# Kernel optimization log

Hardware: AMD Instinct MI355X
Metric: run time of the kernel (lower is better)

The kernel has to match this reference:

```python
import jax, jax.numpy as jnp
import numpy as np

M = 100   # memory_size
D = 512   # memory_dim
B, C, H, W = 4, 512, 64, 64
LN_EPS = 512.0  # nn.LayerNorm(300, 512): 2nd positional arg is eps (faithful quirk)


def _l2norm(x):
    # F.normalize(x, dim=1): x / max(||x||_2, 1e-12)
    return x / jnp.maximum(jnp.linalg.norm(x, axis=1, keepdims=True), 1e-12)


def setup_inputs() -> dict:
    key = jax.random.key(0)
    ks = jax.random.split(key, 16)
    s = 0.03  # weight scale to keep activations sane
    return {
        "fea":    jax.random.normal(ks[0], (B, C, H, W), jnp.float32),
        "item_w": jax.random.normal(ks[1], (D, D), jnp.float32) * 0.02,
        "rel_w":  jax.random.normal(ks[2], (M, D, D), jnp.float32) * 0.02,
        "W1": jax.random.normal(ks[3], (C, D), jnp.float32) * s,  "b1": jnp.zeros((D,), jnp.float32),
        "W2": jax.random.normal(ks[4], (C, D), jnp.float32) * s,  "b2": jnp.zeros((D,), jnp.float32),
        "W3": jax.random.normal(ks[5], (C, M), jnp.float32) * s,  "b3": jnp.zeros((M,), jnp.float32),
        "Wqkv": jax.random.normal(ks[6], (D, 3 * M), jnp.float32) * s, "bqkv": jnp.zeros((3 * M,), jnp.float32),
        "ln_g": jnp.ones((3 * M,), jnp.float32), "ln_b": jnp.zeros((3 * M,), jnp.float32),
        "Wr1": jax.random.normal(ks[7], (D * D, D), jnp.float32) * s, "br1": jnp.zeros((D,), jnp.float32),
        "Wr2": jax.random.normal(ks[8], (M * D, D), jnp.float32) * s, "br2": jnp.zeros((D,), jnp.float32),
    }


def reference(fea, item_w, rel_w, W1, b1, W2, b2, W3, b3,
              Wqkv, bqkv, ln_g, ln_b, Wr1, br1, Wr2, br2):
    b, c, h, w = fea.shape
    x = fea.transpose(0, 2, 3, 1).reshape(b * h * w, c)        # (N, C)
    qn = _l2norm(x)
    ip1 = qn @ W1 + b1                                          # (N, D)
    ip2 = qn @ W2 + b2                                          # (N, D)
    ip3 = jax.nn.softmax(qn @ W3 + b3, axis=-1)                 # (N, M)
    # ip4[b,f] = sum_{n,d} ip3[b,n] ip2[b,d] rel_w[n,d,f]; scan over the M
    # memory slots to avoid an (N, M, D) intermediate.
    def _slot(acc, nw):
        coef, Wn = nw                                           # (N,), (D, D)
        return acc + coef[:, None] * (ip2 @ Wn), None
    ip4, _ = jax.lax.scan(_slot, jnp.zeros_like(ip2), (ip3.T, rel_w))
    # einsum('bd,cf->df', ip4, ip2) == outer(sum_b ip4, sum_c ip2)
    item0 = jnp.outer(ip4.sum(0), ip2.sum(0))                   # (D, D)
    item1 = item_w + ip1.T @ ip1                                # (D, D)
    qkv = (item0 + 1.0 * item1) @ Wqkv + bqkv                   # alpha2=1.0, (D, 3M)
    mu = qkv.mean(-1, keepdims=True)
    var = jnp.var(qkv, axis=-1, keepdims=True)                  # biased, as torch LN
    qkv = (qkv - mu) / jnp.sqrt(var + LN_EPS) * ln_g + ln_b
    q, k, v = qkv[:, :M].T, qkv[:, M:2 * M].T, qkv[:, 2 * M:].T  # each (M, D)
    # op_att: rel0[i,d,f] = sum_j tanh(q[i,d]*k[j,d]) * v[j,f]
    t = jnp.tanh(q[:, None, :] * k[None, :, :])                 # (M, M, D)
    rel0 = jnp.einsum('ijd,jf->idf', t, v)                      # (M, D, D)
    rel_w_new = rel_w + 1.0 * rel0                              # alpha1=1.0
    memory = rel_w_new.reshape(M, D * D) @ Wr1 + br1            # (M, D)
    mn = _l2norm(memory)
    addr = jax.nn.softmax(qn @ mn.T, axis=1)                    # (N, M)
    mf = (addr @ mn).reshape(b, h, w, c).transpose(0, 3, 1, 2)  # (b, C, h, w)
    return jnp.concatenate([fea, mf], axis=1)                   # (b, 2C, h, w)
```

## Files before the change

### kernel.cpp

```cpp
#include <hip/hip_runtime.h>
#include <hip/hip_bf16.h>

#define NTOK 16384
#define DDIM 512
#define MMEM 100
#define HWSZ 4096
#define QKVW 300

typedef __attribute__((ext_vector_type(8))) short short8v;
typedef __attribute__((ext_vector_type(4))) short short4v;
typedef __attribute__((ext_vector_type(4))) float f32x4;

__device__ __forceinline__ unsigned short f2bf(float x) {
  union { __hip_bfloat16 h; unsigned short u; } cv;
  cv.h = __float2bfloat16(x);
  return cv.u;
}
__device__ __forceinline__ float bf2f(unsigned short u) {
  union { unsigned int u; float f; } v; v.u = ((unsigned int)u) << 16;
  return v.f;
}

__global__ __launch_bounds__(256) void cvtw_k(
    const float* __restrict__ W1, const float* __restrict__ W2,
    const float* __restrict__ W3, const float* __restrict__ Wq,
    const float* __restrict__ b1, const float* __restrict__ b2,
    unsigned short* __restrict__ Wcat, unsigned short* __restrict__ o3,
    unsigned short* __restrict__ oq, float* __restrict__ bcat) {
  int idx = blockIdx.x * 256 + threadIdx.x;
  if (idx < 262144) {
    int k = idx >> 9, n = idx & 511;
    Wcat[(size_t)k * 1024 + n] = f2bf(W1[idx]);
    Wcat[(size_t)k * 1024 + 512 + n] = f2bf(W2[idx]);
  } else if (idx < 313344) {
    o3[idx - 262144] = f2bf(W3[idx - 262144]);
  } else if (idx < 466944) {
    oq[idx - 313344] = f2bf(Wq[idx - 313344]);
  } else if (idx < 467968) {
    int i = idx - 466944;
    bcat[i] = (i < 512) ? b1[i] : b2[i - 512];
  }
}

__global__ __launch_bounds__(256) void feat_k(const float* __restrict__ fea,
                                              unsigned short* __restrict__ qnbf,
                                              float* __restrict__ out) {
  __shared__ float tile[512][33];
  __shared__ float psum[8][32];
  __shared__ float invn_s[32];
  const int bid = blockIdx.x;
  const int b = bid >> 7, hw0 = (bid & 127) * 32;
  const int t = threadIdx.x;
  const int hwo = t & 31, cg = t >> 5;
  const float* src = fea + (size_t)b * DDIM * HWSZ + hw0;
  float* dst = out + (size_t)b * (2 * DDIM) * HWSZ + hw0;
  float ss = 0.f;
#pragma unroll 8
  for (int i = 0; i < 64; ++i) {
    int c = cg * 64 + i;
    float v = src[(size_t)c * HWSZ + hwo];
    tile[c][hwo] = v;
    dst[(size_t)c * HWSZ + hwo] = v;
    ss += v * v;
  }
  psum[cg][hwo] = ss;
  __syncthreads();
  if (t < 32) {
    float s = 0.f;
#pragma unroll
    for (int j = 0; j < 8; ++j) s += psum[j][t];
    invn_s[t] = 1.f / fmaxf(sqrtf(s), 1e-12f);
  }
  __syncthreads();
  const int tok = t & 31, c0 = (t >> 5) * 64;
  const float inv = invn_s[tok];
  unsigned short* qp = qnbf + ((size_t)(b * HWSZ + hw0 + tok)) * DDIM + c0;
#pragma unroll
  for (int e8 = 0; e8 < 8; ++e8) {
    short8v p;
#pragma unroll
    for (int e = 0; e < 8; ++e)
      p[e] = (short)f2bf(tile[c0 + e8 * 8 + e][tok] * inv);
    *(short8v*)(qp + e8 * 8) = p;
  }
}

template<bool OUTBF>
__global__ __launch_bounds__(256) void gemm_bf16_k(
    const unsigned short* __restrict__ A, const unsigned short* __restrict__ B,
    const float* __restrict__ bias, void* __restrict__ Cv,
    int M, int N, int K, int lda, int ldb, int ldc) {
  __shared__ unsigned short As[128][40];
  __shared__ unsigned short Bs[32][132];
  const int tid = threadIdx.x;
  const int l = tid & 63, w = tid >> 6;
  const int l15 = l & 15, lhi = l >> 4;
  const int wm = w >> 1, wn = w & 1;
  const int row0 = blockIdx.y * 128, col0 = blockIdx.x * 128;
  const int am = tid >> 1, akq = (tid & 1) << 4;
  const int bk = tid >> 3, bnq = (tid & 7) << 4;
  const int arow = row0 + am;
  f32x4 acc[4][4] = {};

  for (int k0 = 0; k0 < K; k0 += 32) {
    short8v av0 = {}, av1 = {}, bv0 = {}, bv1 = {};
    if (arow < M && k0 + akq < K) {
      const unsigned short* ap = A + (size_t)arow * lda + k0 + akq;
      if (k0 + akq + 15 < K) {
        av0 = *(const short8v*)ap;
        av1 = *(const short8v*)(ap + 8);
      } else {
#pragma unroll
        for (int e = 0; e < 8; ++e) {
          av0[e] = (k0 + akq + e < K) ? (short)ap[e] : (short)0;
          av1[e] = (k0 + akq + 8 + e < K) ? (short)ap[8 + e] : (short)0;
        }
      }
    }
    {
      const int kk = k0 + bk;
      if (kk < K) {
        const unsigned short* bp = B + (size_t)kk * ldb + col0 + bnq;
        if (col0 + bnq + 15 < N) {
          bv0 = *(const short8v*)bp;
          bv1 = *(const short8v*)(bp + 8);
        } else {
#pragma unroll
          for (int e = 0; e < 8; ++e) {
            bv0[e] = (col0 + bnq + e < N) ? (short)bp[e] : (short)0;
            bv1[e] = (col0 + bnq + 8 + e < N) ? (short)bp[8 + e] : (short)0;
          }
        }
      }
    }
    __syncthreads();
    *(short8v*)&As[am][akq] = av0;
    *(short8v*)&As[am][akq + 8] = av1;
    *(short8v*)&Bs[bk][bnq] = bv0;
    *(short8v*)&Bs[bk][bnq + 8] = bv1;
    __syncthreads();
    short8v af[4];
#pragma unroll
    for (int mt = 0; mt < 4; ++mt)
      af[mt] = *(const short8v*)&As[wm * 64 + mt * 16 + l15][lhi * 8];
#pragma unroll
    for (int ct = 0; ct < 4; ++ct) {
      union { short8v v; unsigned short u[8]; } bf;
      const int nn = wn * 64 + ct * 16 + l15;
#pragma unroll
      for (int j = 0; j < 8; ++j) bf.u[j] = Bs[lhi * 8 + j][nn];
#pragma unroll
      for (int mt = 0; mt < 4; ++mt)
        acc[mt][ct] = __builtin_amdgcn_mfma_f32_16x16x32_bf16(
            af[mt], bf.v, acc[mt][ct], 0, 0, 0);
    }
  }

#pragma unroll
  for (int mt = 0; mt < 4; ++mt) {
    const int rb = row0 + wm * 64 + mt * 16 + lhi * 4;
#pragma unroll
    for (int u = 0; u < 4; ++u) {
      const int r = rb + u;
      if (r >= M) continue;
#pragma unroll
      for (int ct = 0; ct < 4; ++ct) {
        const int c = col0 + wn * 64 + ct * 16 + l15;
        if (c >= N) continue;
        float val = acc[mt][ct][u];
        if (bias) val += bias[c];
        if (OUTBF) ((unsigned short*)Cv)[(size_t)r * ldc + c] = f2bf(val);
        else       ((float*)Cv)[(size_t)r * ldc + c] = val;
      }
    }
  }
}

__global__ __launch_bounds__(256) void gemm_sm100_k(
    const unsigned short* __restrict__ A, const unsigned short* __restrict__ B,
    const float* __restrict__ bias, unsigned short* __restrict__ obf,
    int lda, int ldb, int ldo) {
  __shared__ unsigned short As[128][40];
  __shared__ unsigned short Bs[32][132];
  __shared__ float Ps[128][104];
  const int tid = threadIdx.x;
  const int l = tid & 63, w = tid >> 6;
  const int l15 = l & 15, lhi = l >> 4;
  const int wm = w >> 1, wn = w & 1;
  const int row0 = blockIdx.x * 128;
  const int am = tid >> 1, akq = (tid & 1) << 4;
  const int bk = tid >> 3, bnq = (tid & 7) << 4;
  f32x4 acc[4][4] = {};

  for (int k0 = 0; k0 < DDIM; k0 += 32) {
    const unsigned short* ap = A + (size_t)(row0 + am) * lda + k0 + akq;
    short8v av0 = *(const short8v*)ap;
    short8v av1 = *(const short8v*)(ap + 8);
    short8v bv0 = {}, bv1 = {};
    const unsigned short* bp = B + (size_t)(k0 + bk) * ldb + bnq;
    if (bnq + 15 < MMEM) {
      bv0 = *(const short8v*)bp;
      bv1 = *(const short8v*)(bp + 8);
    } else {
#pragma unroll
      for (int e = 0; e < 8; ++e) {
        bv0[e] = (bnq + e < MMEM) ? (short)bp[e] : (short)0;
        bv1[e] = (bnq + 8 + e < MMEM) ? (short)bp[8 + e] : (short)0;
      }
    }
    __syncthreads();
    *(short8v*)&As[am][akq] = av0;
    *(short8v*)&As[am][akq + 8] = av1;
    *(short8v*)&Bs[bk][bnq] = bv0;
    *(short8v*)&Bs[bk][bnq + 8] = bv1;
    __syncthreads();
    short8v af[4];
#pragma unroll
    for (int mt = 0; mt < 4; ++mt)
      af[mt] = *(const short8v*)&As[wm * 64 + mt * 16 + l15][lhi * 8];
#pragma unroll
    for (int ct = 0; ct < 4; ++ct) {
      union { short8v v; unsigned short u[8]; } bf;
      const int nn = wn * 64 + ct * 16 + l15;
#pragma unroll
      for (int j = 0; j < 8; ++j) bf.u[j] = Bs[lhi * 8 + j][nn];
#pragma unroll
      for (int mt = 0; mt < 4; ++mt)
        acc[mt][ct] = __builtin_amdgcn_mfma_f32_16x16x32_bf16(
            af[mt], bf.v, acc[mt][ct], 0, 0, 0);
    }
  }

#pragma unroll
  for (int mt = 0; mt < 4; ++mt) {
#pragma unroll
    for (int u = 0; u < 4; ++u) {
      const int r = wm * 64 + mt * 16 + lhi * 4 + u;
#pragma unroll
      for (int ct = 0; ct < 4; ++ct) {
        const int c = wn * 64 + ct * 16 + l15;
        if (c < MMEM) {
          float val = acc[mt][ct][u];
          if (bias) val += bias[c];
          Ps[r][c] = val;
        }
      }
    }
  }
  __syncthreads();
  for (int rr = 0; rr < 32; ++rr) {
    const int r = w * 32 + rr;
    float v0 = Ps[r][l];
    const bool has1 = (l + 64) < MMEM;
    float v1 = has1 ? Ps[r][l + 64] : -3.4e38f;
    float m = fmaxf(v0, v1);
#pragma unroll
    for (int o = 32; o; o >>= 1) m = fmaxf(m, __shfl_xor(m, o, 64));
    float e0 = expf(v0 - m);
    float e1 = has1 ? expf(v1 - m) : 0.f;
    float s = e0 + e1;
#pragma unroll
    for (int o = 32; o; o >>= 1) s += __shfl_xor(s, o, 64);
    float inv = 1.f / s;
    unsigned short* orow = obf + (size_t)(row0 + r) * ldo;
    orow[l] = f2bf(e0 * inv);
    if (has1) orow[l + 64] = f2bf(e1 * inv);
  }
}

__global__ __launch_bounds__(256) void atb_bf16_k(
    const unsigned short* __restrict__ A, const unsigned short* __restrict__ B,
    float* __restrict__ C, int M, int N, int K,
    int lda, int ldb, int ldc, int KC) {
  __shared__ unsigned short As[128][40];
  __shared__ unsigned short Bs[32][132];
  const int tid = threadIdx.x;
  const int l = tid & 63, w = tid >> 6;
  const int l15 = l & 15, lhi = l >> 4;
  const int wm = w >> 1, wn = w & 1;
  const int row0 = blockIdx.y * 128, col0 = blockIdx.x * 128;
  const int kbeg = blockIdx.z * KC;
  const int kend = min(kbeg + KC, K);
  const int akk = tid >> 3, amq = (tid & 7) << 4;
  const int bk = tid >> 3, bnq = (tid & 7) << 4;
  f32x4 acc[4][4] = {};

  for (int k0 = kbeg; k0 < kend; k0 += 32) {
    unsigned short av[16]; short8v bv0 = {}, bv1 = {};
    {
      const int kk = k0 + akk;
      if (kk < kend) {
        const unsigned short* ap = A + (size_t)kk * lda + row0 + amq;
        if (row0 + amq + 15 < M) {
          *(short8v*)&av[0] = *(const short8v*)ap;
          *(short8v*)&av[8] = *(const short8v*)(ap + 8);
        } else {
#pragma unroll
          for (int e = 0; e < 16; ++e)
            av[e] = (row0 + amq + e < M) ? ap[e] : 0;
        }
      } else {
#pragma unroll
        for (int e = 0; e < 16; ++e) av[e] = 0;
      }
    }
    {
      const int kk = k0 + bk;
      if (kk < kend) {
        const unsigned short* bp = B + (size_t)kk * ldb + col0 + bnq;
        if (col0 + bnq + 15 < N) {
          bv0 = *(const short8v*)bp;
          bv1 = *(const short8v*)(bp + 8);
        } else {
#pragma unroll
          for (int e = 0; e < 8; ++e) {
            bv0[e] = (col0 + bnq + e < N) ? (short)bp[e] : (short)0;
            bv1[e] = (col0 + bnq + 8 + e < N) ? (short)bp[8 + e] : (short)0;
          }
        }
      }
    }
    __syncthreads();
#pragma unroll
    for (int e = 0; e < 16; ++e) As[amq + e][akk] = av[e];
    *(short8v*)&Bs[bk][bnq] = bv0;
    *(short8v*)&Bs[bk][bnq + 8] = bv1;
    __syncthreads();
    short8v af[4];
#pragma unroll
    for (int mt = 0; mt < 4; ++mt)
      af[mt] = *(const short8v*)&As[wm * 64 + mt * 16 + l15][lhi * 8];
#pragma unroll
    for (int ct = 0; ct < 4; ++ct) {
      union { short8v v; unsigned short u[8]; } bf;
      const int nn = wn * 64 + ct * 16 + l15;
#pragma unroll
      for (int j = 0; j < 8; ++j) bf.u[j] = Bs[lhi * 8 + j][nn];
#pragma unroll
      for (int mt = 0; mt < 4; ++mt)
        acc[mt][ct] = __builtin_amdgcn_mfma_f32_16x16x32_bf16(
            af[mt], bf.v, acc[mt][ct], 0, 0, 0);
    }
  }

#pragma unroll
  for (int mt = 0; mt < 4; ++mt) {
    const int rb = row0 + wm * 64 + mt * 16 + lhi * 4;
#pragma unroll
    for (int u = 0; u < 4; ++u) {
      const int r = rb + u;
      if (r >= M) continue;
#pragma unroll
      for (int ct = 0; ct < 4; ++ct) {
        const int c = col0 + wn * 64 + ct * 16 + l15;
        if (c >= N) continue;
        atomicAdd(&C[(size_t)r * ldc + c], acc[mt][ct][u]);
      }
    }
  }
}

__global__ __launch_bounds__(256) void rel0_mfma_k(
    const float* __restrict__ qm, const float* __restrict__ km,
    const float* __restrict__ vm, const float* __restrict__ rel_w,
    unsigned short* __restrict__ relbf) {
  __shared__ unsigned short Ts[128][136];
  __shared__ unsigned short Vs[128][136];
  __shared__ float qv[128];
  const int i = blockIdx.y;
  const int d0 = blockIdx.x * 128;
  const int tid = threadIdx.x;
  const int l = tid & 63, w = tid >> 6;
  const int l15 = l & 15, lhi = l >> 4;
  const int wm = w >> 1, wn = w & 1;

  if (tid < 128) qv[tid] = qm[(size_t)i * DDIM + d0 + tid];
  __syncthreads();
#pragma unroll
  for (int p = 0; p < 8; ++p) {
    int g = p * 2048 + tid * 8;
    int j = g >> 7, dd = g & 127;
    if (j < MMEM) {
      const float* kp = km + (size_t)j * DDIM + d0 + dd;
      float4 k0v = *(const float4*)kp;
      float4 k1v = *(const float4*)(kp + 4);
      float kv[8] = {k0v.x, k0v.y, k0v.z, k0v.w, k1v.x, k1v.y, k1v.z, k1v.w};
#pragma unroll
      for (int e = 0; e < 8; ++e)
        Ts[dd + e][j] = f2bf(tanhf(qv[dd + e] * kv[e]));
    } else {
#pragma unroll
      for (int e = 0; e < 8; ++e) Ts[dd + e][j] = 0;
    }
  }

  for (int f0 = 0; f0 < DDIM; f0 += 128) {
    __syncthreads();
#pragma unroll
    for (int p = 0; p < 8; ++p) {
      int g = p * 2048 + tid * 8;
      int j = g >> 7, ff = g & 127;
      short8v pv;
      if (j < MMEM) {
        const float* vp = vm + (size_t)j * DDIM + f0 + ff;
        float4 v0 = *(const float4*)vp;
        float4 v1 = *(const float4*)(vp + 4);
        pv[0] = (short)f2bf(v0.x); pv[1] = (short)f2bf(v0.y);
        pv[2] = (short)f2bf(v0.z); pv[3] = (short)f2bf(v0.w);
        pv[4] = (short)f2bf(v1.x); pv[5] = (short)f2bf(v1.y);
        pv[6] = (short)f2bf(v1.z); pv[7] = (short)f2bf(v1.w);
      } else {
#pragma unroll
        for (int e = 0; e < 8; ++e) pv[e] = 0;
      }
      *(short8v*)&Vs[j][ff] = pv;
    }
    __syncthreads();
    f32x4 acc[4][4] = {};
#pragma unroll
    for (int ks = 0; ks < 4; ++ks) {
      const int kb = ks * 32;
      short8v af[4];
#pragma unroll
      for (int mt = 0; mt < 4; ++mt)
        af[mt] = *(const short8v*)&Ts[wm * 64 + mt * 16 + l15][kb + lhi * 8];
#pragma unroll
      for (int ct = 0; ct < 4; ++ct) {
        union { short8v v; unsigned short u[8]; } bf;
        const int nn = wn * 64 + ct * 16 + l15;
#pragma unroll
        for (int jj = 0; jj < 8; ++jj) bf.u[jj] = Vs[kb + lhi * 8 + jj][nn];
#pragma unroll
        for (int mt = 0; mt < 4; ++mt)
          acc[mt][ct] = __builtin_amdgcn_mfma_f32_16x16x32_bf16(
              af[mt], bf.v, acc[mt][ct], 0, 0, 0);
      }
    }
#pragma unroll
    for (int mt = 0; mt < 4; ++mt) {
#pragma unroll
      for (int u = 0; u < 4; ++u) {
        const int d = d0 + wm * 64 + mt * 16 + lhi * 4 + u;
        const size_t base = (size_t)i * 262144 + (size_t)d * DDIM;
#pragma unroll
        for (int ct = 0; ct < 4; ++ct) {
          const int f = f0 + wn * 64 + ct * 16 + l15;
          relbf[base + f] = f2bf(rel_w[base + f] + acc[mt][ct][u]);
        }
      }
    }
  }
}

#define MGK 262144
#define MGKC 1024
#define MGCHUNK 256
__global__ __launch_bounds__(1024, 4) void memgemm_k(
    const unsigned short* __restrict__ Ag, const float* __restrict__ Bg,
    float* __restrict__ partial) {
  __shared__ unsigned short As[128][40];
  __shared__ unsigned short Bs[32][520];
  const int tid = threadIdx.x;
  const int l = tid & 63, w = tid >> 6;
  const int l15 = l & 15, lhi = l >> 4;
  const int kbeg = blockIdx.x * MGKC;
  const int arow = tid >> 3, akq = tid & 7;
  const int bk = tid >> 5, bnq = (tid & 31) * 16;
  f32x4 acc[8][2] = {};

  for (int t32 = 0; t32 < MGKC / 32; ++t32) {
    const int kb = kbeg + t32 * 32;
    short4v av = {};
    if (arow < MMEM)
      av = *(const short4v*)(Ag + (size_t)arow * MGK + kb + akq * 4);
    float4 bv[4];
    const float* bp = Bg + (size_t)(kb + bk) * DDIM + bnq;
#pragma unroll
    for (int u = 0; u < 4; ++u) bv[u] = *(const float4*)(bp + 4 * u);
    __syncthreads();
    *(short4v*)&As[arow][akq * 4] = av;
#pragma unroll
    for (int u = 0; u < 2; ++u) {
      short8v pb;
      pb[0] = (short)f2bf(bv[2*u].x);   pb[1] = (short)f2bf(bv[2*u].y);
      pb[2] = (short)f2bf(bv[2*u].z);   pb[3] = (short)f2bf(bv[2*u].w);
      pb[4] = (short)f2bf(bv[2*u+1].x); pb[5] = (short)f2bf(bv[2*u+1].y);
      pb[6] = (short)f2bf(bv[2*u+1].z); pb[7] = (short)f2bf(bv[2*u+1].w);
      *(short8v*)&Bs[bk][bnq + u * 8] = pb;
    }
    __syncthreads();
    union { short8v v; unsigned short u[8]; } bf0, bf1;
    const int nn0 = w * 32 + l15, nn1 = w * 32 + 16 + l15;
#pragma unroll
    for (int j = 0; j < 8; ++j) {
      bf0.u[j] = Bs[lhi * 8 + j][nn0];
      bf1.u[j] = Bs[lhi * 8 + j][nn1];
    }
#pragma unroll
    for (int mt = 0; mt < 8; ++mt) {
      short8v af = *(const short8v*)&As[mt * 16 + l15][lhi * 8];
      acc[mt][0] = __builtin_amdgcn_mfma_f32_16x16x32_bf16(af, bf0.v, acc[mt][0], 0, 0, 0);
      acc[mt][1] = __builtin_amdgcn_mfma_f32_16x16x32_bf16(af, bf1.v, acc[mt][1], 0, 0, 0);
    }
  }

  float* pw = partial + (size_t)blockIdx.x * (MMEM * DDIM);
#pragma unroll
  for (int mt = 0; mt < 8; ++mt) {
    const int r0 = mt * 16 + lhi * 4;
#pragma unroll
    for (int r = 0; r < 4; ++r) {
      const int row = r0 + r;
      if (row < MMEM) {
        pw[(size_t)row * DDIM + w * 32 + l15]      = acc[mt][0][r];
        pw[(size_t)row * DDIM + w * 32 + 16 + l15] = acc[mt][1][r];
      }
    }
  }
}

__global__ __launch_bounds__(512) void reduce_mn_k(
    const float* __restrict__ partial, const float* __restrict__ br1,
    unsigned short* __restrict__ mnbf, unsigned short* __restrict__ mnTbf) {
  __shared__ float r1[8];
  const int i = blockIdx.x, t = threadIdx.x;
  const float* p = partial + (size_t)i * DDIM + t;
  float a0 = 0.f, a1 = 0.f, a2 = 0.f, a3 = 0.f;
  float a4 = 0.f, a5 = 0.f, a6 = 0.f, a7 = 0.f;
  const size_t zs = (size_t)(MMEM * DDIM);
  for (int z = 0; z < MGCHUNK; z += 8) {
    a0 += p[(z + 0) * zs]; a1 += p[(z + 1) * zs];
    a2 += p[(z + 2) * zs]; a3 += p[(z + 3) * zs];
    a4 += p[(z + 4) * zs]; a5 += p[(z + 5) * zs];
    a6 += p[(z + 6) * zs]; a7 += p[(z + 7) * zs];
  }
  float a = br1[t] + ((a0 + a1) + (a2 + a3)) + ((a4 + a5) + (a6 + a7));
  float q = a * a;
#pragma unroll
  for (int o = 32; o; o >>= 1) q += __shfl_xor(q, o, 64);
  if ((t & 63) == 0) r1[t >> 6] = q;
  __syncthreads();
  q = 0.f;
#pragma unroll
  for (int j = 0; j < 8; ++j) q += r1[j];
  float inv = 1.f / fmaxf(sqrtf(q), 1e-12f);
  unsigned short hv = f2bf(a * inv);
  mnbf[(size_t)i * DDIM + t] = hv;
  mnTbf[(size_t)t * MMEM + i] = hv;
}

__global__ __launch_bounds__(512) void colsum_bf_k(const unsigned short* __restrict__ A,
                                                   int ld, float* __restrict__ out) {
  int d = threadIdx.x;
  const unsigned short* p = A + (size_t)blockIdx.x * 64 * ld + d;
  float a0 = 0.f, a1 = 0.f, a2 = 0.f, a3 = 0.f;
  for (int r = 0; r < 64; r += 4) {
    a0 += bf2f(p[(size_t)(r + 0) * ld]);
    a1 += bf2f(p[(size_t)(r + 1) * ld]);
    a2 += bf2f(p[(size_t)(r + 2) * ld]);
    a3 += bf2f(p[(size_t)(r + 3) * ld]);
  }
  atomicAdd(&out[d], (a0 + a1) + (a2 + a3));
}

__global__ __launch_bounds__(256) void ip4sum_k(const float* __restrict__ S,
                                                const float* __restrict__ rel_w,
                                                float* __restrict__ out) {
  __shared__ float sv[64];
  int r0 = blockIdx.x * 64;
  int tid = threadIdx.x;
  if (tid < 64) sv[tid] = S[r0 + tid];
  __syncthreads();
  float a0 = 0.f, a1 = 0.f, a2 = 0.f, a3 = 0.f;
  float b0 = 0.f, b1 = 0.f, b2 = 0.f, b3 = 0.f;
  const float* base = rel_w + (size_t)r0 * DDIM;
  for (int r = 0; r < 64; r += 4) {
    const float* p0 = base + (size_t)(r + 0) * DDIM;
    const float* p1 = base + (size_t)(r + 1) * DDIM;
    const float* p2 = base + (size_t)(r + 2) * DDIM;
    const float* p3 = base + (size_t)(r + 3) * DDIM;
    a0 = fmaf(sv[r + 0], p0[tid], a0); b0 = fmaf(sv[r + 0], p0[tid + 256], b0);
    a1 = fmaf(sv[r + 1], p1[tid], a1); b1 = fmaf(sv[r + 1], p1[tid + 256], b1);
    a2 = fmaf(sv[r + 2], p2[tid], a2); b2 = fmaf(sv[r + 2], p2[tid + 256], b2);
    a3 = fmaf(sv[r + 3], p3[tid], a3); b3 = fmaf(sv[r + 3], p3[tid + 256], b3);
  }
  atomicAdd(&out[tid], (a0 + a1) + (a2 + a3));
  atomicAdd(&out[tid + 256], (b0 + b1) + (b2 + b3));
}

__global__ __launch_bounds__(256) void assemble_item_k(
    const float* __restrict__ item, const float* __restrict__ item_w,
    const float* __restrict__ s4, const float* __restrict__ s2,
    unsigned short* __restrict__ itembf) {
  int idx = blockIdx.x * 256 + threadIdx.x;
  int d = idx >> 9, f = idx & 511;
  itembf[idx] = f2bf(item[idx] + item_w[idx] + s4[d] * s2[f]);
}

__global__ __launch_bounds__(256) void ln300_k(const float* __restrict__ x,
                                               const float* __restrict__ g,
                                               const float* __restrict__ bb,
                                               float* __restrict__ qm,
                                               float* __restrict__ km,
                                               float* __restrict__ vm) {
  __shared__ float r1[4], r2[4];
  int row = blockIdx.x, tid = threadIdx.x;
  const float* xr = x + (size_t)row * QKVW;
  float v1 = xr[tid];
  float v2 = (tid + 256 < QKVW) ? xr[tid + 256] : 0.f;
  float s = v1 + v2, q = v1 * v1 + v2 * v2;
#pragma unroll
  for (int o = 32; o; o >>= 1) { s += __shfl_xor(s, o, 64); q += __shfl_xor(q, o, 64); }
  if ((tid & 63) == 0) { r1[tid >> 6] = s; r2[tid >> 6] = q; }
  __syncthreads();
  s = r1[0] + r1[1] + r1[2] + r1[3];
  q = r2[0] + r2[1] + r2[2] + r2[3];
  float mean = s * (1.f / 300.f);
  float var = q * (1.f / 300.f) - mean * mean;
  float inv = rsqrtf(var + 512.0f);
  float y1 = (v1 - mean) * inv * g[tid] + bb[tid];
  int j = tid;
  if (j < 100)      qm[(size_t)j * DDIM + row] = y1;
  else if (j < 200) km[(size_t)(j - 100) * DDIM + row] = y1;
  else              vm[(size_t)(j - 200) * DDIM + row] = y1;
  if (tid + 256 < QKVW) {
    float y2 = (v2 - mean) * inv * g[tid + 256] + bb[tid + 256];
    vm[(size_t)(tid + 56) * DDIM + row] = y2;
  }
}

__global__ void write_mf_k(const unsigned short* __restrict__ mfbf,
                           float* __restrict__ out) {
  __shared__ float tile[32][33];
  int b = blockIdx.z, hw0 = blockIdx.x * 32, c0 = blockIdx.y * 32;
  int tx = threadIdx.x, ty = threadIdx.y;
#pragma unroll
  for (int i = 0; i < 32; i += 8)
    tile[ty + i][tx] =
        bf2f(mfbf[((size_t)b * HWSZ + hw0 + ty + i) * DDIM + c0 + tx]);
  __syncthreads();
#pragma unroll
  for (int i = 0; i < 32; i += 8)
    out[(size_t)b * 4194304 + (size_t)(512 + c0 + ty + i) * HWSZ + hw0 + tx] =
        tile[tx][ty + i];
}

extern "C" void kernel_launch(void* const* d_in, const int* in_sizes, int n_in,
                              void* d_out, int out_size, void* d_ws, size_t ws_size,
                              hipStream_t stream) {
  (void)in_sizes; (void)n_in; (void)out_size; (void)ws_size;
  const float* fea    = (const float*)d_in[0];
  const float* item_w = (const float*)d_in[1];
  const float* rel_w  = (const float*)d_in[2];
  const float* W1     = (const float*)d_in[3];
  const float* b1     = (const float*)d_in[4];
  const float* W2     = (const float*)d_in[5];
  const float* b2     = (const float*)d_in[6];
  const float* W3     = (const float*)d_in[7];
  const float* b3     = (const float*)d_in[8];
  const float* Wqkv   = (const float*)d_in[9];
  const float* bqkv   = (const float*)d_in[10];
  const float* ln_g   = (const float*)d_in[11];
  const float* ln_b   = (const float*)d_in[12];
  const float* Wr1    = (const float*)d_in[13];
  const float* br1    = (const float*)d_in[14];
  float* out = (float*)d_out;
  float* ws = (float*)d_ws;

  float* S       = ws;
  float* ip4sum  = S       + 51200;
  float* ip2sum  = ip4sum  + 512;
  float* item    = ip2sum  + 512;
  float* qkv     = item    + 262144;
  float* qm      = qkv     + 153600;
  float* km      = qm      + 51200;
  float* vm      = km      + 51200;
  float* bcat    = vm      + 51200;
  float* partial = bcat    + 1024;
  unsigned short* u16base = (unsigned short*)(partial + 13107200);
  unsigned short* qnbf    = u16base;
  unsigned short* ip12bf  = qnbf    + 8388608;
  unsigned short* ip3bf   = ip12bf  + 16777216;
  unsigned short* addrbf  = ip3bf   + 1638400;
  unsigned short* relbf   = addrbf  + 2097152;
  unsigned short* mfbf    = relbf   + 26214400;
  unsigned short* itembf  = mfbf    + 8388608;
  unsigned short* mnbf    = itembf  + 262144;
  unsigned short* mnTbf   = mnbf    + 51200;
  unsigned short* Wcat    = mnTbf   + 51200;
  unsigned short* W3bf    = Wcat    + 524288;
  unsigned short* Wqbf    = W3bf    + 51200;

  hipMemsetAsync(S, 0, (size_t)(51200 + 512 + 512 + 262144) * sizeof(float), stream);

  cvtw_k<<<1828, 256, 0, stream>>>(W1, W2, W3, Wqkv, b1, b2, Wcat, W3bf, Wqbf, bcat);

  feat_k<<<512, 256, 0, stream>>>(fea, qnbf, out);

  gemm_bf16_k<true><<<dim3(8, 128), 256, 0, stream>>>(
      qnbf, Wcat, bcat, ip12bf, NTOK, 1024, DDIM, DDIM, 1024, 1024);
  gemm_sm100_k<<<128, 256, 0, stream>>>(qnbf, W3bf, b3, ip3bf, DDIM, MMEM, MMEM);

  atb_bf16_k<<<dim3(4, 4, 16), 256, 0, stream>>>(
      ip12bf, ip12bf, item, DDIM, DDIM, NTOK, 1024, 1024, DDIM, 1024);
  atb_bf16_k<<<dim3(4, 1, 16), 256, 0, stream>>>(
      ip3bf, ip12bf + 512, S, MMEM, DDIM, NTOK, MMEM, 1024, DDIM, 1024);
  colsum_bf_k<<<256, 512, 0, stream>>>(ip12bf + 512, 1024, ip2sum);
  ip4sum_k<<<800, 256, 0, stream>>>(S, rel_w, ip4sum);

  assemble_item_k<<<1024, 256, 0, stream>>>(item, item_w, ip4sum, ip2sum, itembf);

  gemm_bf16_k<false><<<dim3(3, 4), 256, 0, stream>>>(
      itembf, Wqbf, bqkv, qkv, DDIM, QKVW, DDIM, DDIM, QKVW, QKVW);
  ln300_k<<<512, 256, 0, stream>>>(qkv, ln_g, ln_b, qm, km, vm);

  rel0_mfma_k<<<dim3(4, MMEM), 256, 0, stream>>>(qm, km, vm, rel_w, relbf);

  memgemm_k<<<dim3(MGCHUNK), 1024, 0, stream>>>(relbf, Wr1, partial);
  reduce_mn_k<<<MMEM, 512, 0, stream>>>(partial, br1, mnbf, mnTbf);

  gemm_sm100_k<<<128, 256, 0, stream>>>(qnbf, mnTbf, nullptr, addrbf, DDIM, MMEM, 128);
  gemm_bf16_k<true><<<dim3(4, 128), 256, 0, stream>>>(
      addrbf, mnbf, nullptr, mfbf, NTOK, DDIM, MMEM, 128, DDIM, DDIM);

  write_mf_k<<<dim3(128, 16, 4), dim3(32, 8), 0, stream>>>(mfbf, out);
}
```

Baseline: 582.1 us.

## Fuse weight conversion into feature kernel, fold item assembly into QKV GEMM, swizzle LDS

Merges the weight-to-bf16 conversion kernel into the feature-normalisation kernel as extra blocks, removing one launch. It also folds the item assembly (item + item_w + outer product) into the A-tile load of a dedicated QKV GEMM, which drops the itembf buffer and one launch. The split-K factor of the two A^T·B reductions is doubled or quadrupled to put more blocks in flight, at the cost of more atomic accumulation. In memgemm the B tile gets an XOR swizzle and the A tile extra padding to cut LDS bank conflicts.

```diff
diff --git a/kernel.cpp b/kernel.cpp
--- a/kernel.cpp
+++ b/kernel.cpp
@@ -21,30 +21,32 @@
   return v.f;
 }
 
-__global__ __launch_bounds__(256) void cvtw_k(
+__global__ __launch_bounds__(256) void feat_cvtw_k(
+    const float* __restrict__ fea, unsigned short* __restrict__ qnbf,
+    float* __restrict__ out,
     const float* __restrict__ W1, const float* __restrict__ W2,
     const float* __restrict__ W3, const float* __restrict__ Wq,
     const float* __restrict__ b1, const float* __restrict__ b2,
     unsigned short* __restrict__ Wcat, unsigned short* __restrict__ o3,
     unsigned short* __restrict__ oq, float* __restrict__ bcat) {
-  int idx = blockIdx.x * 256 + threadIdx.x;
-  if (idx < 262144) {
-    int k = idx >> 9, n = idx & 511;
-    Wcat[(size_t)k * 1024 + n] = f2bf(W1[idx]);
-    Wcat[(size_t)k * 1024 + 512 + n] = f2bf(W2[idx]);
-  } else if (idx < 313344) {
-    o3[idx - 262144] = f2bf(W3[idx - 262144]);
-  } else if (idx < 466944) {
-    oq[idx - 313344] = f2bf(Wq[idx - 313344]);
-  } else if (idx < 467968) {
-    int i = idx - 466944;
-    bcat[i] = (i < 512) ? b1[i] : b2[i - 512];
-  }
-}
-
-__global__ __launch_bounds__(256) void feat_k(const float* __restrict__ fea,
-                                              unsigned short* __restrict__ qnbf,
-                                              float* __restrict__ out) {
+  if (blockIdx.x >= 512) {
+    int base = (blockIdx.x - 512) * 256 + threadIdx.x;
+    for (int idx = base; idx < 467968; idx += 229 * 256) {
+      if (idx < 262144) {
+        int k = idx >> 9, n = idx & 511;
+        Wcat[(size_t)k * 1024 + n] = f2bf(W1[idx]);
+        Wcat[(size_t)k * 1024 + 512 + n] = f2bf(W2[idx]);
+      } else if (idx < 313344) {
+        o3[idx - 262144] = f2bf(W3[idx - 262144]);
+      } else if (idx < 466944) {
+        oq[idx - 313344] = f2bf(Wq[idx - 313344]);
+      } else {
+        int i = idx - 466944;
+        bcat[i] = (i < 512) ? b1[i] : b2[i - 512];
+      }
+    }
+    return;
+  }
   __shared__ float tile[512][33];
   __shared__ float psum[8][32];
   __shared__ float invn_s[32];
@@ -176,6 +178,100 @@
   }
 }
 
+__global__ __launch_bounds__(256) void gemm_qkv_k(
+    const float* __restrict__ item, const float* __restrict__ item_w,
+    const float* __restrict__ s4, const float* __restrict__ s2,
+    const unsigned short* __restrict__ B, const float* __restrict__ bias,
+    float* __restrict__ C) {
+  __shared__ unsigned short As[128][40];
+  __shared__ unsigned short Bs[32][132];
+  const int tid = threadIdx.x;
+  const int l = tid & 63, w = tid >> 6;
+  const int l15 = l & 15, lhi = l >> 4;
+  const int wm = w >> 1, wn = w & 1;
+  const int row0 = blockIdx.y * 128, col0 = blockIdx.x * 128;
+  const int am = tid >> 1, akq = (tid & 1) << 4;
+  const int bk = tid >> 3, bnq = (tid & 7) << 4;
+  const int arow = row0 + am;
+  f32x4 acc[4][4] = {};
+
+  for (int k0 = 0; k0 < DDIM; k0 += 32) {
+    float av[16];
+    {
+      const size_t off = (size_t)arow * DDIM + k0 + akq;
+      const float s4r = s4[arow];
+#pragma unroll
+      for (int u = 0; u < 4; ++u) {
+        float4 a = *(const float4*)(item + off + 4 * u);
+        float4 b = *(const float4*)(item_w + off + 4 * u);
+        float4 c = *(const float4*)(s2 + k0 + akq + 4 * u);
+        av[4*u+0] = a.x + b.x + s4r * c.x;
+        av[4*u+1] = a.y + b.y + s4r * c.y;
+        av[4*u+2] = a.z + b.z + s4r * c.z;
+        av[4*u+3] = a.w + b.w + s4r * c.w;
+      }
+    }
+    short8v bv0 = {}, bv1 = {};
+    {
+      const int kk = k0 + bk;
+      const unsigned short* bp = B + (size_t)kk * QKVW + col0 + bnq;
+      if (col0 + bnq + 15 < QKVW) {
+        bv0 = *(const short8v*)bp;
+        bv1 = *(const short8v*)(bp + 8);
+      } else {
+#pragma unroll
+        for (int e = 0; e < 8; ++e) {
+          bv0[e] = (col0 + bnq + e < QKVW) ? (short)bp[e] : (short)0;
+          bv1[e] = (col0 + bnq + 8 + e < QKVW) ? (short)bp[8 + e] : (short)0;
+        }
+      }
+    }
+    __syncthreads();
+    {
+      short8v p0, p1;
+#pragma unroll
+      for (int e = 0; e < 8; ++e) p0[e] = (short)f2bf(av[e]);
+#pragma unroll
+      for (int e = 0; e < 8; ++e) p1[e] = (short)f2bf(av[8 + e]);
+      *(short8v*)&As[am][akq] = p0;
+      *(short8v*)&As[am][akq + 8] = p1;
+    }
+    *(short8v*)&Bs[bk][bnq] = bv0;
+    *(short8v*)&Bs[bk][bnq + 8] = bv1;
+    __syncthreads();
+    short8v af[4];
+#pragma unroll
+    for (int mt = 0; mt < 4; ++mt)
+      af[mt] = *(const short8v*)&As[wm * 64 + mt * 16 + l15][lhi * 8];
+#pragma unroll
+    for (int ct = 0; ct < 4; ++ct) {
+      union { short8v v; unsigned short u[8]; } bf;
+      const int nn = wn * 64 + ct * 16 + l15;
+#pragma unroll
+      for (int j = 0; j < 8; ++j) bf.u[j] = Bs[lhi * 8 + j][nn];
+#pragma unroll
+      for (int mt = 0; mt < 4; ++mt)
+        acc[mt][ct] = __builtin_amdgcn_mfma_f32_16x16x32_bf16(
+            af[mt], bf.v, acc[mt][ct], 0, 0, 0);
+    }
+  }
+
+#pragma unroll
+  for (int mt = 0; mt < 4; ++mt) {
+    const int rb = row0 + wm * 64 + mt * 16 + lhi * 4;
+#pragma unroll
+    for (int u = 0; u < 4; ++u) {
+      const int r = rb + u;
+#pragma unroll
+      for (int ct = 0; ct < 4; ++ct) {
+        const int c = col0 + wn * 64 + ct * 16 + l15;
+        if (c >= QKVW) continue;
+        C[(size_t)r * QKVW + c] = acc[mt][ct][u] + bias[c];
+      }
+    }
+  }
+}
+
 __global__ __launch_bounds__(256) void gemm_sm100_k(
     const unsigned short* __restrict__ A, const unsigned short* __restrict__ B,
     const float* __restrict__ bias, unsigned short* __restrict__ obf,
@@ -458,7 +554,7 @@
 __global__ __launch_bounds__(1024, 4) void memgemm_k(
     const unsigned short* __restrict__ Ag, const float* __restrict__ Bg,
     float* __restrict__ partial) {
-  __shared__ unsigned short As[128][40];
+  __shared__ unsigned short As[128][44];
   __shared__ unsigned short Bs[32][520];
   const int tid = threadIdx.x;
   const int l = tid & 63, w = tid >> 6;
@@ -466,6 +562,8 @@
   const int kbeg = blockIdx.x * MGKC;
   const int arow = tid >> 3, akq = tid & 7;
   const int bk = tid >> 5, bnq = (tid & 31) * 16;
+  const int bsw = ((bk >> 3) & 3) << 4;
+  const int csw = lhi << 4;
   f32x4 acc[8][2] = {};
 
   for (int t32 = 0; t32 < MGKC / 32; ++t32) {
@@ -486,15 +584,15 @@
       pb[2] = (short)f2bf(bv[2*u].z);   pb[3] = (short)f2bf(bv[2*u].w);
       pb[4] = (short)f2bf(bv[2*u+1].x); pb[5] = (short)f2bf(bv[2*u+1].y);
       pb[6] = (short)f2bf(bv[2*u+1].z); pb[7] = (short)f2bf(bv[2*u+1].w);
-      *(short8v*)&Bs[bk][bnq + u * 8] = pb;
+      *(short8v*)&Bs[bk][(bnq + u * 8) ^ bsw] = pb;
     }
     __syncthreads();
     union { short8v v; unsigned short u[8]; } bf0, bf1;
     const int nn0 = w * 32 + l15, nn1 = w * 32 + 16 + l15;
 #pragma unroll
     for (int j = 0; j < 8; ++j) {
-      bf0.u[j] = Bs[lhi * 8 + j][nn0];
-      bf1.u[j] = Bs[lhi * 8 + j][nn1];
+      bf0.u[j] = Bs[lhi * 8 + j][nn0 ^ csw];
+      bf1.u[j] = Bs[lhi * 8 + j][nn1 ^ csw];
     }
 #pragma unroll
     for (int mt = 0; mt < 8; ++mt) {
@@ -586,15 +684,6 @@
   }
   atomicAdd(&out[tid], (a0 + a1) + (a2 + a3));
   atomicAdd(&out[tid + 256], (b0 + b1) + (b2 + b3));
-}
-
-__global__ __launch_bounds__(256) void assemble_item_k(
-    const float* __restrict__ item, const float* __restrict__ item_w,
-    const float* __restrict__ s4, const float* __restrict__ s2,
-    unsigned short* __restrict__ itembf) {
-  int idx = blockIdx.x * 256 + threadIdx.x;
-  int d = idx >> 9, f = idx & 511;
-  itembf[idx] = f2bf(item[idx] + item_w[idx] + s4[d] * s2[f]);
 }
 
 __global__ __launch_bounds__(256) void ln300_k(const float* __restrict__ x,
@@ -684,8 +773,7 @@
   unsigned short* addrbf  = ip3bf   + 1638400;
   unsigned short* relbf   = addrbf  + 2097152;
   unsigned short* mfbf    = relbf   + 26214400;
-  unsigned short* itembf  = mfbf    + 8388608;
-  unsigned short* mnbf    = itembf  + 262144;
+  unsigned short* mnbf    = mfbf    + 8388608;
   unsigned short* mnTbf   = mnbf    + 51200;
   unsigned short* Wcat    = mnTbf   + 51200;
   unsigned short* W3bf    = Wcat    + 524288;
@@ -693,25 +781,22 @@
 
   hipMemsetAsync(S, 0, (size_t)(51200 + 512 + 512 + 262144) * sizeof(float), stream);
 
-  cvtw_k<<<1828, 256, 0, stream>>>(W1, W2, W3, Wqkv, b1, b2, Wcat, W3bf, Wqbf, bcat);
-
-  feat_k<<<512, 256, 0, stream>>>(fea, qnbf, out);
+  feat_cvtw_k<<<741, 256, 0, stream>>>(fea, qnbf, out, W1, W2, W3, Wqkv,
+                                       b1, b2, Wcat, W3bf, Wqbf, bcat);
 
   gemm_bf16_k<true><<<dim3(8, 128), 256, 0, stream>>>(
       qnbf, Wcat, bcat, ip12bf, NTOK, 1024, DDIM, DDIM, 1024, 1024);
   gemm_sm100_k<<<128, 256, 0, stream>>>(qnbf, W3bf, b3, ip3bf, DDIM, MMEM, MMEM);
 
-  atb_bf16_k<<<dim3(4, 4, 16), 256, 0, stream>>>(
-      ip12bf, ip12bf, item, DDIM, DDIM, NTOK, 1024, 1024, DDIM, 1024);
-  atb_bf16_k<<<dim3(4, 1, 16), 256, 0, stream>>>(
-      ip3bf, ip12bf + 512, S, MMEM, DDIM, NTOK, MMEM, 1024, DDIM, 1024);
+  atb_bf16_k<<<dim3(4, 4, 32), 256, 0, stream>>>(
+      ip12bf, ip12bf, item, DDIM, DDIM, NTOK, 1024, 1024, DDIM, 512);
+  atb_bf16_k<<<dim3(4, 1, 64), 256, 0, stream>>>(
+      ip3bf, ip12bf + 512, S, MMEM, DDIM, NTOK, MMEM, 1024, DDIM, 256);
   colsum_bf_k<<<256, 512, 0, stream>>>(ip12bf + 512, 1024, ip2sum);
   ip4sum_k<<<800, 256, 0, stream>>>(S, rel_w, ip4sum);
 
-  assemble_item_k<<<1024, 256, 0, stream>>>(item, item_w, ip4sum, ip2sum, itembf);
-
-  gemm_bf16_k<false><<<dim3(3, 4), 256, 0, stream>>>(
-      itembf, Wqbf, bqkv, qkv, DDIM, QKVW, DDIM, DDIM, QKVW, QKVW);
+  gemm_qkv_k<<<dim3(3, 4), 256, 0, stream>>>(item, item_w, ip4sum, ip2sum,
+                                             Wqbf, bqkv, qkv);
   ln300_k<<<512, 256, 0, stream>>>(qkv, ln_g, ln_b, qm, km, vm);
 
   rel0_mfma_k<<<dim3(4, MMEM), 256, 0, stream>>>(qm, km, vm, rel_w, relbf);
```

Result: faster. 554.4 us (-4.8%).
